# Optimization experiments

Hardware: AMD Instinct MI355X
Metric: run time of the kernel (lower is better)

The kernel has to match this reference:

```python
import jax, jax.numpy as jnp
import numpy as np
import math

N_NODES = 50000
N_EDGES = 800000
F_IN = 32
HID = 64


def _layernorm(x, g, b, eps=1e-5):
    mu = x.mean(-1, keepdims=True)
    var = ((x - mu) ** 2).mean(-1, keepdims=True)
    return (x - mu) / jnp.sqrt(var + eps) * g + b


def _tconv(x, src, dst, Wq, bq, Wk, bk, Wv, bv, Ws, heads):
    # PyG TransformerConv (concat=True, root_weight=True, bias=False on skip)
    N = x.shape[0]
    C = Wq.shape[1] // heads
    q = (x @ Wq + bq).reshape(N, heads, C)[dst]  # [E,H,C] gathered at targets
    k = (x @ Wk + bk).reshape(N, heads, C)[src]  # [E,H,C] gathered at sources
    v = (x @ Wv + bv).reshape(N, heads, C)[src]
    scores = (q * k).sum(-1) / math.sqrt(C)      # [E,H]
    m = jax.ops.segment_max(scores, dst, num_segments=N)   # [N,H]
    p = jnp.exp(scores - m[dst])
    denom = jax.ops.segment_sum(p, dst, num_segments=N)
    alpha = p / (denom[dst] + 1e-16)             # segment softmax over in-edges
    agg = jax.ops.segment_sum(v * alpha[..., None], dst, num_segments=N)
    return agg.reshape(N, heads * C) + x @ Ws    # + skip (no bias)


def setup_inputs() -> dict:
    key = jax.random.key(0)
    ks = iter(jax.random.split(key, 64))
    def rn(shape, s=0.1):
        return jax.random.normal(next(ks), shape, jnp.float32) * s
    inp = {
        "x": rn((N_NODES, F_IN), 1.0),
        "edge_index": jax.random.randint(next(ks), (2, N_EDGES), 0, N_NODES, dtype=jnp.int32),
        "ln0_g": jnp.ones((F_IN,), jnp.float32),
        "ln0_b": jnp.zeros((F_IN,), jnp.float32),
    }
    dims = [F_IN, HID, HID]
    for l in range(3):
        d = dims[l]
        inp[f"Wq{l}"] = rn((d, HID)); inp[f"bq{l}"] = rn((HID,), 0.05)
        inp[f"Wk{l}"] = rn((d, HID)); inp[f"bk{l}"] = rn((HID,), 0.05)
        inp[f"Wv{l}"] = rn((d, HID)); inp[f"bv{l}"] = rn((HID,), 0.05)
        inp[f"Ws{l}"] = rn((d, HID))
        inp[f"g{l}"] = jnp.ones((HID,), jnp.float32)
        inp[f"b{l}"] = jnp.zeros((HID,), jnp.float32)
    inp["Wr1"] = rn((HID, HID // 2)); inp["br1"] = jnp.zeros((HID // 2,), jnp.float32)
    inp["Wr2"] = rn((HID // 2, 1));   inp["br2"] = jnp.zeros((1,), jnp.float32)
    inp["Wt1"] = rn((HID, HID // 2)); inp["bt1"] = jnp.zeros((HID // 2,), jnp.float32)
    inp["Wt2"] = rn((HID // 2, 1));   inp["bt2"] = jnp.zeros((1,), jnp.float32)
    return inp


def reference(x, edge_index, ln0_g, ln0_b,
              Wq0, bq0, Wk0, bk0, Wv0, bv0, Ws0, g0, b0,
              Wq1, bq1, Wk1, bk1, Wv1, bv1, Ws1, g1, b1,
              Wq2, bq2, Wk2, bk2, Wv2, bv2, Ws2, g2, b2,
              Wr1, br1, Wr2, br2, Wt1, bt1, Wt2, bt2):
    src, dst = edge_index[0], edge_index[1]
    h = _layernorm(x, ln0_g, ln0_b)
    layers = [
        (Wq0, bq0, Wk0, bk0, Wv0, bv0, Ws0, g0, b0, 4),
        (Wq1, bq1, Wk1, bk1, Wv1, bv1, Ws1, g1, b1, 4),
        (Wq2, bq2, Wk2, bk2, Wv2, bv2, Ws2, g2, b2, 1),
    ]
    for i, (Wq, bq, Wk, bk, Wv, bv, Ws, g, b, heads) in enumerate(layers):
        x_res = h if h.shape[-1] == HID else None
        h = _tconv(h, src, dst, Wq, bq, Wk, bk, Wv, bv, Ws, heads)
        h = _layernorm(h, g, b)
        if x_res is not None and i > 0:
            h = h + 0.1 * x_res
        if i < len(layers) - 1:
            h = jax.nn.relu(h)  # dropout is identity in eval mode
    rtt = jax.nn.relu(h @ Wr1 + br1) @ Wr2 + br2      # [N,1]
    retrans = jax.nn.relu(h @ Wt1 + bt1) @ Wt2 + bt2  # [N,1]
    return jnp.concatenate([rtt, retrans], axis=1)    # [N,2]
```

## Files before the change

kernel.cpp:

```cpp
#include <hip/hip_runtime.h>
#include <hip/hip_bf16.h>
#include <hip/hip_fp16.h>
#include <math.h>

#define N_NODES 50000
#define N_EDGES 800000
#define HID 64
#define NBK 196
#define EPB 1024
#define SB  ((N_EDGES + EPB - 1) / EPB)
#define FLAT (NBK * SB)
#define SCAN_B ((FLAT + 255) / 256)

#define QKVS0_BLKS 3125

#define LN0_BLKS   6250
#define HIST_BLKS  SB
#define WP0_BLKS   32
#define WP12_BLKS  64
#define PREP_BLKS  (LN0_BLKS + HIST_BLKS + WP0_BLKS + 2 * WP12_BLKS)

typedef __attribute__((ext_vector_type(8))) short short8;
typedef __attribute__((ext_vector_type(4))) float float4v;
typedef __attribute__((ext_vector_type(2))) float float2v;

__device__ __forceinline__ unsigned short f32_to_bf16_rne(float f) {
    unsigned int u = __float_as_uint(f);
    unsigned int r = u + 0x7fffu + ((u >> 16) & 1u);
    return (unsigned short)(r >> 16);
}

__device__ __forceinline__ unsigned int f32_to_fp8_byte(float f) {
    return (unsigned int)__builtin_amdgcn_cvt_pk_fp8_f32(f, f, 0, false) & 0xffu;
}
template <bool HI>
__device__ __forceinline__ float2v fp8x2_to_f32(unsigned int w) {
    return __builtin_amdgcn_cvt_pk_f32_fp8((int)w, HI);
}
__device__ __forceinline__ float2 h2_to_f32(unsigned int w) {
    __half2 h = *reinterpret_cast<__half2*>(&w);
    return __half22float2(h);
}

__device__ __forceinline__ void ln0_body(int b, int t,
        const float* __restrict__ x, const float* __restrict__ g,
        const float* __restrict__ bb, float* __restrict__ h0) {
    int lane = t & 63;
    int n = b * 8 + (t >> 6) * 2 + (lane >> 5);
    int c = lane & 31;
    float v = x[n * 32 + c];
    float s = v;
    #pragma unroll
    for (int off = 1; off < 32; off <<= 1) s += __shfl_xor(s, off);
    float mu = s * (1.0f / 32.0f);
    float d = v - mu;
    float vs = d * d;
    #pragma unroll
    for (int off = 1; off < 32; off <<= 1) vs += __shfl_xor(vs, off);
    float var = vs * (1.0f / 32.0f);
    h0[n * 32 + c] = d * rsqrtf(var + 1e-5f) * g[c] + bb[c];
}

__device__ __forceinline__ void wprep_body(int idx, int KS,
        const float* __restrict__ Wq, const float* __restrict__ Wk,
        const float* __restrict__ Wv, const float* __restrict__ Ws,
        unsigned short* __restrict__ Wp) {
    int j = idx & 7;
    int lane = (idx >> 3) & 63;
    int ts = idx >> 9;
    int s = ts % KS;
    int tile = ts / KS;
    int which = tile >> 2;
    int slice = tile & 3;
    int k = s * 32 + ((lane >> 4) * 8) + j;
    int col = slice * 16 + (lane & 15);
    const float* W = (which == 0) ? Wq : (which == 1) ? Wk : (which == 2) ? Wv : Ws;
    Wp[idx] = f32_to_bf16_rne(W[k * 64 + col]);
}

__global__ __launch_bounds__(256) void prep_kernel(
        const float* __restrict__ x, const float* __restrict__ ln0g,
        const float* __restrict__ ln0b, float* __restrict__ h0,
        const int* __restrict__ dst, int* __restrict__ ghist,
        const float* __restrict__ Wq0, const float* __restrict__ Wk0,
        const float* __restrict__ Wv0, const float* __restrict__ Ws0,
        unsigned short* __restrict__ Wp0,
        const float* __restrict__ Wq1, const float* __restrict__ Wk1,
        const float* __restrict__ Wv1, const float* __restrict__ Ws1,
        unsigned short* __restrict__ Wp1,
        const float* __restrict__ Wq2, const float* __restrict__ Wk2,
        const float* __restrict__ Wv2, const float* __restrict__ Ws2,
        unsigned short* __restrict__ Wp2) {
    __shared__ int hist[NBK];
    int b = blockIdx.x;
    int t = threadIdx.x;
    if (b < LN0_BLKS) {
        ln0_body(b, t, x, ln0g, ln0b, h0);
    } else if (b < LN0_BLKS + HIST_BLKS) {
        int i = b - LN0_BLKS;
        for (int k = t; k < NBK; k += 256) hist[k] = 0;
        __syncthreads();
        int e0 = i * EPB;
        #pragma unroll
        for (int r = 0; r < EPB / 256; r++) {
            int e = e0 + r * 256 + t;
            if (e < N_EDGES) atomicAdd(&hist[dst[e] >> 8], 1);
        }
        __syncthreads();
        for (int k = t; k < NBK; k += 256) ghist[k * SB + i] = hist[k];
    } else if (b < LN0_BLKS + HIST_BLKS + WP0_BLKS) {
        int idx = (b - LN0_BLKS - HIST_BLKS) * 256 + t;
        wprep_body(idx, 1, Wq0, Wk0, Wv0, Ws0, Wp0);
    } else if (b < LN0_BLKS + HIST_BLKS + WP0_BLKS + WP12_BLKS) {
        int idx = (b - LN0_BLKS - HIST_BLKS - WP0_BLKS) * 256 + t;
        wprep_body(idx, 2, Wq1, Wk1, Wv1, Ws1, Wp1);
    } else {
        int idx = (b - LN0_BLKS - HIST_BLKS - WP0_BLKS - WP12_BLKS) * 256 + t;
        wprep_body(idx, 2, Wq2, Wk2, Wv2, Ws2, Wp2);
    }
}

__global__ void scan1_kernel(const int* __restrict__ ghist, int* __restrict__ csum) {
    int f = blockIdx.x * 256 + threadIdx.x;
    int v = (f < FLAT) ? ghist[f] : 0;
    #pragma unroll
    for (int off = 1; off < 64; off <<= 1) v += __shfl_xor(v, off);
    __shared__ int ws[4];
    if ((threadIdx.x & 63) == 0) ws[threadIdx.x >> 6] = v;
    __syncthreads();
    if (threadIdx.x == 0) csum[blockIdx.x] = ws[0] + ws[1] + ws[2] + ws[3];
}

__global__ void scan2_kernel(const int* __restrict__ csum, int* __restrict__ coff,
                             int* __restrict__ bbase, int* __restrict__ row_ptr) {
    int lane = threadIdx.x;
    int carry = 0;
    for (int base = 0; base < SCAN_B; base += 64) {
        int i = base + lane;
        int v = (i < SCAN_B) ? csum[i] : 0;
        int incl = v;
        #pragma unroll
        for (int off = 1; off < 64; off <<= 1) {
            int tt = __shfl_up(incl, off);
            if (lane >= off) incl += tt;
        }
        if (i < SCAN_B) coff[i] = carry + incl - v;
        carry += __shfl(incl, 63);
    }
    if (lane == 0) { bbase[NBK] = N_EDGES; row_ptr[N_NODES] = N_EDGES; }
}

__global__ void scan3_kernel(const int* __restrict__ ghist, const int* __restrict__ coff,
                             int* __restrict__ goff, int* __restrict__ bbase) {
    int f = blockIdx.x * 256 + threadIdx.x;
    int lane = threadIdx.x & 63;
    int w = threadIdx.x >> 6;
    int v = (f < FLAT) ? ghist[f] : 0;
    int incl = v;
    #pragma unroll
    for (int off = 1; off < 64; off <<= 1) {
        int tt = __shfl_up(incl, off);
        if (lane >= off) incl += tt;
    }
    __shared__ int ws[4];
    if (lane == 63) ws[w] = incl;
    __syncthreads();
    int woff = 0;
    #pragma unroll
    for (int k = 0; k < 4; k++) if (k < w) woff += ws[k];
    int excl = coff[blockIdx.x] + woff + incl - v;
    if (f < FLAT) {
        goff[f] = excl;
        if (f % SB == 0) bbase[f / SB] = excl;
    }
}

template <int D>
__device__ __forceinline__ void qkvs_body(int bid, int t,
        const float* __restrict__ h,
        const unsigned short* __restrict__ Wp,
        const float* __restrict__ bq, const float* __restrict__ bk,
        const float* __restrict__ bv, float scale,
        float* __restrict__ Qf, float* __restrict__ Sf,
        unsigned int* __restrict__ K8, uint2* __restrict__ Vh) {
    constexpr int KS = D / 32;
    int lane = t & 63;
    int w = t >> 6;
    int n0 = bid * 16;
    int n16 = lane & 15;
    int quad = lane >> 4;
    int col = w * 16 + n16;

    short8 afrag[KS];
    #pragma unroll
    for (int s = 0; s < KS; s++) {
        const float* hp = &h[(n0 + n16) * D + s * 32 + quad * 8];
        float4 a0 = *(const float4*)hp;
        float4 a1 = *(const float4*)(hp + 4);
        short8 af;
        af[0] = (short)f32_to_bf16_rne(a0.x);
        af[1] = (short)f32_to_bf16_rne(a0.y);
        af[2] = (short)f32_to_bf16_rne(a0.z);
        af[3] = (short)f32_to_bf16_rne(a0.w);
        af[4] = (short)f32_to_bf16_rne(a1.x);
        af[5] = (short)f32_to_bf16_rne(a1.y);
        af[6] = (short)f32_to_bf16_rne(a1.z);
        af[7] = (short)f32_to_bf16_rne(a1.w);
        afrag[s] = af;
    }

    float4v accs[4];
    #pragma unroll
    for (int which = 0; which < 4; which++) {
        float4v acc = {0.0f, 0.0f, 0.0f, 0.0f};
        int tile = which * 4 + w;
        #pragma unroll
        for (int s = 0; s < KS; s++) {
            short8 bfrag = *(const short8*)&Wp[((tile * KS + s) * 64 + lane) * 8];
            acc = __builtin_amdgcn_mfma_f32_16x16x32_bf16(afrag[s], bfrag, acc, 0, 0, 0);
        }
        accs[which] = acc;
    }

    float bqc = bq[col], bkc = bk[col], bvc = bv[col];
    int j = n16 & 3;
    int mword = (col >> 2);

    #pragma unroll
    for (int r = 0; r < 4; r++) {
        int node = n0 + quad * 4 + r;
        Qf[node * 64 + col] = (accs[0][r] + bqc) * scale;
        Sf[node * 64 + col] = accs[3][r];
        unsigned int ku = f32_to_fp8_byte(accs[1][r] + bkc) << (8 * j);
        ku |= __shfl_xor(ku, 1); ku |= __shfl_xor(ku, 2);
        unsigned int hb = (unsigned int)__half_as_ushort(__float2half_rn(accs[2][r] + bvc));
        unsigned int vx = (j < 2) ? (hb << (16 * j)) : 0u;
        unsigned int vy = (j >= 2) ? (hb << (16 * (j - 2))) : 0u;
        vx |= __shfl_xor(vx, 1); vx |= __shfl_xor(vx, 2);
        vy |= __shfl_xor(vy, 1); vy |= __shfl_xor(vy, 2);
        if (j == 0) {
            K8[node * 16 + mword] = ku;
            Vh[node * 16 + mword] = make_uint2(vx, vy);
        }
    }
}

template <int D>
__global__ __launch_bounds__(256) void qkvs_mfma_kernel(
        const float* __restrict__ h,
        const unsigned short* __restrict__ Wp,
        const float* __restrict__ bq, const float* __restrict__ bk,
        const float* __restrict__ bv, float scale,
        float* __restrict__ Qf, float* __restrict__ Sf,
        unsigned int* __restrict__ K8, uint2* __restrict__ Vh) {
    qkvs_body<D>(blockIdx.x, threadIdx.x, h, Wp, bq, bk, bv, scale, Qf, Sf, K8, Vh);
}

__global__ __launch_bounds__(256) void scatter_qkvs0_kernel(
        const int* __restrict__ src, const int* __restrict__ dst,
        const int* __restrict__ goff, int2* __restrict__ ebkt,
        const float* __restrict__ h, const unsigned short* __restrict__ Wp,
        const float* __restrict__ bq, const float* __restrict__ bk,
        const float* __restrict__ bv, float scale,
        float* __restrict__ Qf, float* __restrict__ Sf,
        unsigned int* __restrict__ K8, uint2* __restrict__ Vh) {
    __shared__ int hist[NBK];
    int t = threadIdx.x;
    if (blockIdx.x < SB) {
        int i = blockIdx.x;
        for (int k = t; k < NBK; k += 256) hist[k] = 0;
        __syncthreads();
        int e0 = i * EPB;
        #pragma unroll
        for (int r = 0; r < EPB / 256; r++) {
            int e = e0 + r * 256 + t;
            if (e < N_EDGES) {
                int s = src[e], d = dst[e];
                int k = d >> 8;
                int rank = atomicAdd(&hist[k], 1);
                ebkt[goff[k * SB + i] + rank] = make_int2(s, d);
            }
        }
    } else {
        qkvs_body<32>(blockIdx.x - SB, t, h, Wp, bq, bk, bv, scale, Qf, Sf, K8, Vh);
    }
}

__global__ __launch_bounds__(256) void bucket_build_kernel(
        const int2* __restrict__ ebkt, const int* __restrict__ bbase,
        int* __restrict__ row_ptr, int* __restrict__ colb) {
    __shared__ int ldeg[256];
    __shared__ int lcur[256];
    __shared__ int wsum[4];
    int b = blockIdx.x;
    int t = threadIdx.x;
    int cbase = bbase[b];
    int cnt = bbase[b + 1] - cbase;

    ldeg[t] = 0;
    __syncthreads();
    for (int i = t; i < cnt; i += 256) {
        int2 e = ebkt[cbase + i];
        atomicAdd(&ldeg[e.y & 255], 1);
    }
    __syncthreads();

    int lane = t & 63;
    int w = t >> 6;
    int v = ldeg[t];
    int incl = v;
    #pragma unroll
    for (int off = 1; off < 64; off <<= 1) {
        int tt = __shfl_up(incl, off);
        if (lane >= off) incl += tt;
    }
    if (lane == 63) wsum[w] = incl;
    __syncthreads();
    int woff = 0;
    #pragma unroll
    for (int k = 0; k < 4; k++) if (k < w) woff += wsum[k];
    int excl = woff + incl - v;

    int node = b * 256 + t;
    if (node < N_NODES) row_ptr[node] = cbase + excl;
    lcur[t] = excl;
    __syncthreads();

    for (int i = t; i < cnt; i += 256) {
        int2 e = ebkt[cbase + i];
        int r = atomicAdd(&lcur[e.y & 255], 1);
        colb[cbase + r] = e.x;
    }
}

template <int HEADS, bool RES, bool RELU, bool HEAD>
__global__ __launch_bounds__(256) void agg_kernel(
                           const float* __restrict__ Qf,
                           const float* __restrict__ Sf,
                           const unsigned int* __restrict__ K8,
                           const uint2* __restrict__ Vh,
                           const int* __restrict__ row_ptr, const int* __restrict__ colb,
                           const float* __restrict__ g, const float* __restrict__ b,
                           const float* __restrict__ h_in, float* __restrict__ h_out,
                           const float* __restrict__ Wr1, const float* __restrict__ br1,
                           const float* __restrict__ Wr2, const float* __restrict__ br2,
                           const float* __restrict__ Wt1, const float* __restrict__ bt1,
                           const float* __restrict__ Wt2, const float* __restrict__ bt2,
                           float* __restrict__ out) {
    constexpr int C = HID / HEADS;
    int lane = threadIdx.x & 63;
    int m = lane & 15;
    int grp = lane >> 4;
    int n = blockIdx.x * 4 + (threadIdx.x >> 6);

    float4 q4 = *(const float4*)&Qf[n * 64 + 4 * m];

    int beg = row_ptr[n], end = row_ptr[n + 1];

    float ssum = 0.0f;
    float acc0 = 0.0f, acc1 = 0.0f, acc2 = 0.0f, acc3 = 0.0f;

    for (int i0 = beg + grp; i0 < end; i0 += 8) {
        #pragma unroll
        for (int u = 0; u < 2; u++) {
            int idx = i0 + u * 4;
            bool ok = idx < end;
            int s = ok ? colb[idx] : 0;
            unsigned int kw = K8[(size_t)s * 16 + m];
            uint2 vw = Vh[(size_t)s * 16 + m];

            float2v ka = fp8x2_to_f32<false>(kw);
            float2v kb = fp8x2_to_f32<true>(kw);
            float t = fmaf(q4.x, ka.x, fmaf(q4.y, ka.y,
                      fmaf(q4.z, kb.x, q4.w * kb.y)));
            #pragma unroll
            for (int off = 1; off < C / 4; off <<= 1) t += __shfl_xor(t, off);
            float pv = ok ? __expf(t) : 0.0f;
            ssum += pv;

            float2 v0 = h2_to_f32(vw.x), v1 = h2_to_f32(vw.y);
            acc0 = fmaf(pv, v0.x, acc0);
            acc1 = fmaf(pv, v0.y, acc1);
            acc2 = fmaf(pv, v1.x, acc2);
            acc3 = fmaf(pv, v1.y, acc3);
        }
    }

    #pragma unroll
    for (int off = 16; off < 64; off <<= 1) {
        ssum += __shfl_xor(ssum, off);
        acc0 += __shfl_xor(acc0, off);
        acc1 += __shfl_xor(acc1, off);
        acc2 += __shfl_xor(acc2, off);
        acc3 += __shfl_xor(acc3, off);
    }

    float inv = 1.0f / (ssum + 1e-16f);
    float4 sv = *(const float4*)&Sf[n * 64 + 4 * m];
    float o0 = fmaf(acc0, inv, sv.x);
    float o1 = fmaf(acc1, inv, sv.y);
    float o2 = fmaf(acc2, inv, sv.z);
    float o3 = fmaf(acc3, inv, sv.w);

    float s = (o0 + o1) + (o2 + o3);
    #pragma unroll
    for (int off = 1; off < 16; off <<= 1) s += __shfl_xor(s, off);
    float mu = s * (1.0f / 64.0f);
    float d0 = o0 - mu, d1 = o1 - mu, d2 = o2 - mu, d3 = o3 - mu;
    float vs = (d0 * d0 + d1 * d1) + (d2 * d2 + d3 * d3);
    #pragma unroll
    for (int off = 1; off < 16; off <<= 1) vs += __shfl_xor(vs, off);
    float rstd = rsqrtf(vs * (1.0f / 64.0f) + 1e-5f);

    float4 gv = *(const float4*)&g[4 * m];
    float4 bv = *(const float4*)&b[4 * m];
    float y0 = d0 * rstd * gv.x + bv.x;
    float y1 = d1 * rstd * gv.y + bv.y;
    float y2 = d2 * rstd * gv.z + bv.z;
    float y3 = d3 * rstd * gv.w + bv.w;
    if (RES) {
        float4 rv = *(const float4*)&h_in[n * 64 + 4 * m];
        y0 = fmaf(0.1f, rv.x, y0);
        y1 = fmaf(0.1f, rv.y, y1);
        y2 = fmaf(0.1f, rv.z, y2);
        y3 = fmaf(0.1f, rv.w, y3);
    }
    if (RELU) {
        y0 = fmaxf(y0, 0.0f); y1 = fmaxf(y1, 0.0f);
        y2 = fmaxf(y2, 0.0f); y3 = fmaxf(y3, 0.0f);
    }

    if (!HEAD) {
        if (grp == 0) {
            float4 yv = make_float4(y0, y1, y2, y3);
            *(float4*)&h_out[n * 64 + 4 * m] = yv;
        }
    } else {
        __shared__ float sh[4][HID];
        int wave = threadIdx.x >> 6;
        if (grp == 0) {
            float4 yv = make_float4(y0, y1, y2, y3);
            *(float4*)&sh[wave][4 * m] = yv;
        }
        __syncthreads();
        int half = lane >> 5;
        int j = lane & 31;
        const float* W1 = half ? Wt1 : Wr1;
        const float* b1 = half ? bt1 : br1;
        const float* W2 = half ? Wt2 : Wr2;
        const float* b2v = half ? bt2 : br2;
        float a = b1[j];
        #pragma unroll 8
        for (int i = 0; i < 64; i++) a = fmaf(sh[wave][i], W1[i * 32 + j], a);
        a = fmaxf(a, 0.0f);
        float r = a * W2[j];
        #pragma unroll
        for (int off = 1; off < 32; off <<= 1) r += __shfl_xor(r, off);
        if (j == 0) out[n * 2 + half] = r + b2v[0];
    }
}

extern "C" void kernel_launch(void* const* d_in, const int* in_sizes, int n_in,
                              void* d_out, int out_size, void* d_ws, size_t ws_size,
                              hipStream_t stream) {
    const float* x    = (const float*)d_in[0];
    const int*   ei   = (const int*)d_in[1];
    const int*   src  = ei;
    const int*   dst  = ei + N_EDGES;
    const float* ln0g = (const float*)d_in[2];
    const float* ln0b = (const float*)d_in[3];

    const float* P[27];
    for (int i = 0; i < 27; i++) P[i] = (const float*)d_in[4 + i];
    const float* Wr1 = (const float*)d_in[31];
    const float* br1 = (const float*)d_in[32];
    const float* Wr2 = (const float*)d_in[33];
    const float* br2 = (const float*)d_in[34];
    const float* Wt1 = (const float*)d_in[35];
    const float* bt1 = (const float*)d_in[36];
    const float* Wt2 = (const float*)d_in[37];
    const float* bt2 = (const float*)d_in[38];

    float* out = (float*)d_out;

    float* hbuf0 = (float*)d_ws;
    float* hbuf1 = hbuf0 + N_NODES * 64;
    float* Qf    = hbuf1 + N_NODES * 64;
    float* Sf    = Qf + N_NODES * 64;
    unsigned int* K8 = (unsigned int*)(Sf + N_NODES * 64);
    uint2* Vh    = (uint2*)(K8 + N_NODES * 16);
    int* row_ptr = (int*)(Vh + N_NODES * 16);
    int* colb    = row_ptr + (N_NODES + 1);
    int* ghist   = colb + N_EDGES;
    int* goff    = ghist + FLAT;
    int* csum    = goff + FLAT;
    int* coff    = csum + SCAN_B;
    int* bbase   = coff + SCAN_B;
    unsigned short* Wp0 = (unsigned short*)(bbase + NBK + 1);
    unsigned short* Wp1 = Wp0 + 16 * 1 * 512;
    unsigned short* Wp2 = Wp1 + 16 * 2 * 512;
    int2* ebkt = (int2*)hbuf1;

    prep_kernel<<<PREP_BLKS, 256, 0, stream>>>(x, ln0g, ln0b, hbuf0,
        dst, ghist,
        P[0],  P[2],  P[4],  P[6],  Wp0,
        P[9],  P[11], P[13], P[15], Wp1,
        P[18], P[20], P[22], P[24], Wp2);
    scan1_kernel<<<SCAN_B, 256, 0, stream>>>(ghist, csum);
    scan2_kernel<<<1, 64, 0, stream>>>(csum, coff, bbase, row_ptr);
    scan3_kernel<<<SCAN_B, 256, 0, stream>>>(ghist, coff, goff, bbase);
    scatter_qkvs0_kernel<<<SB + QKVS0_BLKS, 256, 0, stream>>>(src, dst, goff, ebkt,
        hbuf0, Wp0, P[1], P[3], P[5], 0.25f, Qf, Sf, K8, Vh);
    bucket_build_kernel<<<NBK, 256, 0, stream>>>(ebkt, bbase, row_ptr, colb);

    agg_kernel<4, false, true, false><<<12500, 256, 0, stream>>>(Qf, Sf, K8, Vh,
        row_ptr, colb, P[7], P[8], nullptr, hbuf1,
        Wr1, br1, Wr2, br2, Wt1, bt1, Wt2, bt2, out);

    qkvs_mfma_kernel<64><<<3125, 256, 0, stream>>>(hbuf1, Wp1,
        P[10], P[12], P[14], 0.25f, Qf, Sf, K8, Vh);
    agg_kernel<4, true, true, false><<<12500, 256, 0, stream>>>(Qf, Sf, K8, Vh,
        row_ptr, colb, P[16], P[17], hbuf1, hbuf0,
        Wr1, br1, Wr2, br2, Wt1, bt1, Wt2, bt2, out);

    qkvs_mfma_kernel<64><<<3125, 256, 0, stream>>>(hbuf0, Wp2,
        P[19], P[21], P[23], 0.125f, Qf, Sf, K8, Vh);
    agg_kernel<1, true, false, true><<<12500, 256, 0, stream>>>(Qf, Sf, K8, Vh,
        row_ptr, colb, P[25], P[26], hbuf0, hbuf1,
        Wr1, br1, Wr2, br2, Wt1, bt1, Wt2, bt2, out);
}
```

Baseline: 362.5 us.

## Pack Q and skip as bf16 pairs and use one lane per channel

Q and the skip projection are now stored as bf16 halves of a single 32-bit word per channel, replacing two fp32 arrays and halving that write and read traffic. The aggregation kernel is restructured so each of the 64 lanes owns one channel and walks the edges serially, eight at a time. K and V are read as byte and half-word gathers per lane. This replaces the old layout where four lane groups each handled a different edge with four channels per lane. The cost is more cross-lane shuffles and exp evaluations per edge, and bf16 rounding of the queries and skip term could affect accuracy.

```diff
diff --git a/kernel.cpp b/kernel.cpp
--- a/kernel.cpp
+++ b/kernel.cpp
@@ -181,7 +181,7 @@
         const unsigned short* __restrict__ Wp,
         const float* __restrict__ bq, const float* __restrict__ bk,
         const float* __restrict__ bv, float scale,
-        float* __restrict__ Qf, float* __restrict__ Sf,
+        unsigned int* __restrict__ QS,
         unsigned int* __restrict__ K8, uint2* __restrict__ Vh) {
     constexpr int KS = D / 32;
     int lane = t & 63;
@@ -229,8 +229,9 @@
     #pragma unroll
     for (int r = 0; r < 4; r++) {
         int node = n0 + quad * 4 + r;
-        Qf[node * 64 + col] = (accs[0][r] + bqc) * scale;
-        Sf[node * 64 + col] = accs[3][r];
+        unsigned int qw = f32_to_bf16_rne((accs[0][r] + bqc) * scale);
+        unsigned int sw = f32_to_bf16_rne(accs[3][r]);
+        QS[node * 64 + col] = (sw << 16) | qw;
         unsigned int ku = f32_to_fp8_byte(accs[1][r] + bkc) << (8 * j);
         ku |= __shfl_xor(ku, 1); ku |= __shfl_xor(ku, 2);
         unsigned int hb = (unsigned int)__half_as_ushort(__float2half_rn(accs[2][r] + bvc));
@@ -251,9 +252,9 @@
         const unsigned short* __restrict__ Wp,
         const float* __restrict__ bq, const float* __restrict__ bk,
         const float* __restrict__ bv, float scale,
-        float* __restrict__ Qf, float* __restrict__ Sf,
+        unsigned int* __restrict__ QS,
         unsigned int* __restrict__ K8, uint2* __restrict__ Vh) {
-    qkvs_body<D>(blockIdx.x, threadIdx.x, h, Wp, bq, bk, bv, scale, Qf, Sf, K8, Vh);
+    qkvs_body<D>(blockIdx.x, threadIdx.x, h, Wp, bq, bk, bv, scale, QS, K8, Vh);
 }
 
 __global__ __launch_bounds__(256) void scatter_qkvs0_kernel(
@@ -262,7 +263,7 @@
         const float* __restrict__ h, const unsigned short* __restrict__ Wp,
         const float* __restrict__ bq, const float* __restrict__ bk,
         const float* __restrict__ bv, float scale,
-        float* __restrict__ Qf, float* __restrict__ Sf,
+        unsigned int* __restrict__ QS,
         unsigned int* __restrict__ K8, uint2* __restrict__ Vh) {
     __shared__ int hist[NBK];
     int t = threadIdx.x;
@@ -282,7 +283,7 @@
             }
         }
     } else {
-        qkvs_body<32>(blockIdx.x - SB, t, h, Wp, bq, bk, bv, scale, Qf, Sf, K8, Vh);
+        qkvs_body<32>(blockIdx.x - SB, t, h, Wp, bq, bk, bv, scale, QS, K8, Vh);
     }
 }
 
@@ -335,10 +336,9 @@
 
 template <int HEADS, bool RES, bool RELU, bool HEAD>
 __global__ __launch_bounds__(256) void agg_kernel(
-                           const float* __restrict__ Qf,
-                           const float* __restrict__ Sf,
-                           const unsigned int* __restrict__ K8,
-                           const uint2* __restrict__ Vh,
+                           const unsigned int* __restrict__ QS,
+                           const unsigned char* __restrict__ K8b,
+                           const unsigned short* __restrict__ Vhs,
                            const int* __restrict__ row_ptr, const int* __restrict__ colb,
                            const float* __restrict__ g, const float* __restrict__ b,
                            const float* __restrict__ h_in, float* __restrict__ h_out,
@@ -347,101 +347,58 @@
                            const float* __restrict__ Wt1, const float* __restrict__ bt1,
                            const float* __restrict__ Wt2, const float* __restrict__ bt2,
                            float* __restrict__ out) {
-    constexpr int C = HID / HEADS;
     int lane = threadIdx.x & 63;
-    int m = lane & 15;
-    int grp = lane >> 4;
     int n = blockIdx.x * 4 + (threadIdx.x >> 6);
 
-    float4 q4 = *(const float4*)&Qf[n * 64 + 4 * m];
+    unsigned int qsw = QS[(size_t)n * 64 + lane];
+    float q = __uint_as_float(qsw << 16);
 
     int beg = row_ptr[n], end = row_ptr[n + 1];
 
-    float ssum = 0.0f;
-    float acc0 = 0.0f, acc1 = 0.0f, acc2 = 0.0f, acc3 = 0.0f;
-
-    for (int i0 = beg + grp; i0 < end; i0 += 8) {
-        #pragma unroll
-        for (int u = 0; u < 2; u++) {
-            int idx = i0 + u * 4;
+    float ssum = 0.0f, acc = 0.0f;
+
+    for (int e0 = beg; e0 < end; e0 += 8) {
+        #pragma unroll
+        for (int u = 0; u < 8; u++) {
+            int idx = e0 + u;
             bool ok = idx < end;
-            int s = ok ? colb[idx] : 0;
-            unsigned int kw = K8[(size_t)s * 16 + m];
-            uint2 vw = Vh[(size_t)s * 16 + m];
-
-            float2v ka = fp8x2_to_f32<false>(kw);
-            float2v kb = fp8x2_to_f32<true>(kw);
-            float t = fmaf(q4.x, ka.x, fmaf(q4.y, ka.y,
-                      fmaf(q4.z, kb.x, q4.w * kb.y)));
+            int ic = ok ? idx : (end - 1);
+            int s = colb[ic];
+            float k = fp8x2_to_f32<false>((unsigned)K8b[(size_t)s * 64 + lane]).x;
+            float v = h2_to_f32((unsigned)Vhs[(size_t)s * 64 + lane]).x;
+            float t = q * k;
             #pragma unroll
-            for (int off = 1; off < C / 4; off <<= 1) t += __shfl_xor(t, off);
-            float pv = ok ? __expf(t) : 0.0f;
-            ssum += pv;
-
-            float2 v0 = h2_to_f32(vw.x), v1 = h2_to_f32(vw.y);
-            acc0 = fmaf(pv, v0.x, acc0);
-            acc1 = fmaf(pv, v0.y, acc1);
-            acc2 = fmaf(pv, v1.x, acc2);
-            acc3 = fmaf(pv, v1.y, acc3);
-        }
-    }
-
-    #pragma unroll
-    for (int off = 16; off < 64; off <<= 1) {
-        ssum += __shfl_xor(ssum, off);
-        acc0 += __shfl_xor(acc0, off);
-        acc1 += __shfl_xor(acc1, off);
-        acc2 += __shfl_xor(acc2, off);
-        acc3 += __shfl_xor(acc3, off);
+            for (int off = 1; off < (HEADS == 4 ? 16 : 64); off <<= 1)
+                t += __shfl_xor(t, off);
+            float p = ok ? __expf(t) : 0.0f;
+            ssum += p;
+            acc = fmaf(p, v, acc);
+        }
     }
 
     float inv = 1.0f / (ssum + 1e-16f);
-    float4 sv = *(const float4*)&Sf[n * 64 + 4 * m];
-    float o0 = fmaf(acc0, inv, sv.x);
-    float o1 = fmaf(acc1, inv, sv.y);
-    float o2 = fmaf(acc2, inv, sv.z);
-    float o3 = fmaf(acc3, inv, sv.w);
-
-    float s = (o0 + o1) + (o2 + o3);
-    #pragma unroll
-    for (int off = 1; off < 16; off <<= 1) s += __shfl_xor(s, off);
+    float o = fmaf(acc, inv, __uint_as_float(qsw & 0xffff0000u));
+
+    float s = o;
+    #pragma unroll
+    for (int off = 1; off < 64; off <<= 1) s += __shfl_xor(s, off);
     float mu = s * (1.0f / 64.0f);
-    float d0 = o0 - mu, d1 = o1 - mu, d2 = o2 - mu, d3 = o3 - mu;
-    float vs = (d0 * d0 + d1 * d1) + (d2 * d2 + d3 * d3);
-    #pragma unroll
-    for (int off = 1; off < 16; off <<= 1) vs += __shfl_xor(vs, off);
+    float d = o - mu;
+    float vs = d * d;
+    #pragma unroll
+    for (int off = 1; off < 64; off <<= 1) vs += __shfl_xor(vs, off);
     float rstd = rsqrtf(vs * (1.0f / 64.0f) + 1e-5f);
 
-    float4 gv = *(const float4*)&g[4 * m];
-    float4 bv = *(const float4*)&b[4 * m];
-    float y0 = d0 * rstd * gv.x + bv.x;
-    float y1 = d1 * rstd * gv.y + bv.y;
-    float y2 = d2 * rstd * gv.z + bv.z;
-    float y3 = d3 * rstd * gv.w + bv.w;
-    if (RES) {
-        float4 rv = *(const float4*)&h_in[n * 64 + 4 * m];
-        y0 = fmaf(0.1f, rv.x, y0);
-        y1 = fmaf(0.1f, rv.y, y1);
-        y2 = fmaf(0.1f, rv.z, y2);
-        y3 = fmaf(0.1f, rv.w, y3);
-    }
-    if (RELU) {
-        y0 = fmaxf(y0, 0.0f); y1 = fmaxf(y1, 0.0f);
-        y2 = fmaxf(y2, 0.0f); y3 = fmaxf(y3, 0.0f);
-    }
+    float y = d * rstd * g[lane] + b[lane];
+    if (RES) y = fmaf(0.1f, h_in[(size_t)n * 64 + lane], y);
+    if (RELU) y = fmaxf(y, 0.0f);
 
     if (!HEAD) {
-        if (grp == 0) {
-            float4 yv = make_float4(y0, y1, y2, y3);
-            *(float4*)&h_out[n * 64 + 4 * m] = yv;
-        }
+        h_out[(size_t)n * 64 + lane] = y;
     } else {
         __shared__ float sh[4][HID];
         int wave = threadIdx.x >> 6;
-        if (grp == 0) {
-            float4 yv = make_float4(y0, y1, y2, y3);
-            *(float4*)&sh[wave][4 * m] = yv;
-        }
+        sh[wave][lane] = y;
         __syncthreads();
         int half = lane >> 5;
         int j = lane & 31;
@@ -485,9 +442,8 @@
 
     float* hbuf0 = (float*)d_ws;
     float* hbuf1 = hbuf0 + N_NODES * 64;
-    float* Qf    = hbuf1 + N_NODES * 64;
-    float* Sf    = Qf + N_NODES * 64;
-    unsigned int* K8 = (unsigned int*)(Sf + N_NODES * 64);
+    unsigned int* QSb = (unsigned int*)(hbuf1 + N_NODES * 64);
+    unsigned int* K8 = QSb + N_NODES * 64;
     uint2* Vh    = (uint2*)(K8 + N_NODES * 16);
     int* row_ptr = (int*)(Vh + N_NODES * 16);
     int* colb    = row_ptr + (N_NODES + 1);
@@ -510,22 +466,25 @@
     scan2_kernel<<<1, 64, 0, stream>>>(csum, coff, bbase, row_ptr);
     scan3_kernel<<<SCAN_B, 256, 0, stream>>>(ghist, coff, goff, bbase);
     scatter_qkvs0_kernel<<<SB + QKVS0_BLKS, 256, 0, stream>>>(src, dst, goff, ebkt,
-        hbuf0, Wp0, P[1], P[3], P[5], 0.25f, Qf, Sf, K8, Vh);
+        hbuf0, Wp0, P[1], P[3], P[5], 0.25f, QSb, K8, Vh);
     bucket_build_kernel<<<NBK, 256, 0, stream>>>(ebkt, bbase, row_ptr, colb);
 
-    agg_kernel<4, false, true, false><<<12500, 256, 0, stream>>>(Qf, Sf, K8, Vh,
+    agg_kernel<4, false, true, false><<<12500, 256, 0, stream>>>(QSb,
+        (const unsigned char*)K8, (const unsigned short*)Vh,
         row_ptr, colb, P[7], P[8], nullptr, hbuf1,
         Wr1, br1, Wr2, br2, Wt1, bt1, Wt2, bt2, out);
 
     qkvs_mfma_kernel<64><<<3125, 256, 0, stream>>>(hbuf1, Wp1,
-        P[10], P[12], P[14], 0.25f, Qf, Sf, K8, Vh);
-    agg_kernel<4, true, true, false><<<12500, 256, 0, stream>>>(Qf, Sf, K8, Vh,
+        P[10], P[12], P[14], 0.25f, QSb, K8, Vh);
+    agg_kernel<4, true, true, false><<<12500, 256, 0, stream>>>(QSb,
+        (const unsigned char*)K8, (const unsigned short*)Vh,
         row_ptr, colb, P[16], P[17], hbuf1, hbuf0,
         Wr1, br1, Wr2, br2, Wt1, bt1, Wt2, bt2, out);
 
     qkvs_mfma_kernel<64><<<3125, 256, 0, stream>>>(hbuf0, Wp2,
-        P[19], P[21], P[23], 0.125f, Qf, Sf, K8, Vh);
-    agg_kernel<1, true, false, true><<<12500, 256, 0, stream>>>(Qf, Sf, K8, Vh,
+        P[19], P[21], P[23], 0.125f, QSb, K8, Vh);
+    agg_kernel<1, true, false, true><<<12500, 256, 0, stream>>>(QSb,
+        (const unsigned char*)K8, (const unsigned short*)Vh,
         row_ptr, colb, P[25], P[26], hbuf0, hbuf1,
         Wr1, br1, Wr2, br2, Wt1, bt1, Wt2, bt2, out);
 }
```

Result: slower. 402.7 us (+11.1%).
